# Kernel tuning notes

Measured on AMD Instinct MI355X. Metric: run time of the kernel, lower is better.

The kernel has to match this reference:

```python
import jax, jax.numpy as jnp
import numpy as np
import math

IN_CH = 512
OUT_CH = 512
KSIZE = 3
W_DIM = 512
CONV_SCALE = 1.0 / math.sqrt(IN_CH * KSIZE * KSIZE)
MOD_SCALE = 1.0 / math.sqrt(W_DIM)


def setup_inputs() -> dict:
    key = jax.random.key(0)
    k1, k2, k3, k4 = jax.random.split(key, 4)
    B, H, W = 16, 64, 64
    return {
        "input": jax.random.normal(k1, (B, IN_CH, H, W), dtype=jnp.float32),
        "style": jax.random.normal(k2, (B, W_DIM), dtype=jnp.float32),
        "weight": jax.random.normal(k3, (1, OUT_CH, IN_CH, KSIZE, KSIZE), dtype=jnp.float32),
        "mod_weight": jax.random.normal(k4, (IN_CH, W_DIM), dtype=jnp.float32),
        "mod_bias": jnp.ones((IN_CH,), dtype=jnp.float32),
    }


def reference(input, style, weight, mod_weight, mod_bias):
    B, Cin, H, Wd = input.shape
    # EqualLinear modulation: style -> per-sample, per-input-channel scale
    s = style @ (mod_weight * MOD_SCALE).T + mod_bias  # [B, Cin]
    s = s[:, None, :, None, None]                      # [B,1,Cin,1,1]
    w = CONV_SCALE * weight * s                        # [B,Cout,Cin,k,k]
    demod = jax.lax.rsqrt(jnp.sum(w * w, axis=(2, 3, 4)) + 1e-8)  # [B,Cout]
    w = w * demod[:, :, None, None, None]
    # Grouped conv with groups=batch, same as torch F.conv2d
    w = w.reshape(B * OUT_CH, Cin, KSIZE, KSIZE)
    x = input.reshape(1, B * Cin, H, Wd)
    pad = KSIZE // 2
    out = jax.lax.conv_general_dilated(
        x, w,
        window_strides=(1, 1),
        padding=[(pad, pad), (pad, pad)],
        dimension_numbers=("NCHW", "OIHW", "NCHW"),
        feature_group_count=B,
    )
    return out.reshape(B, OUT_CH, out.shape[2], out.shape[3])
```

## Files before the change

kernel.cpp:

```cpp
#include <hip/hip_runtime.h>
#include <hip/hip_bf16.h>


constexpr float CONV_SCALE = 0.014731391274719738f;
constexpr float MOD_SCALE  = 0.04419417382415922f;

typedef short  bf16x8 __attribute__((ext_vector_type(8)));
typedef float  f32x4  __attribute__((ext_vector_type(4)));

__device__ __forceinline__ unsigned short f2bf(float f) {
  unsigned u = __float_as_uint(f);
  u += 0x7fffu + ((u >> 16) & 1u);
  return (unsigned short)(u >> 16);
}

__device__ __forceinline__ void async16(const void* g, void* l) {
  __builtin_amdgcn_global_load_lds((const __attribute__((address_space(1))) unsigned int*)g,
                                   (__attribute__((address_space(3))) unsigned int*)l,
                                   16, 0, 0);
}

__global__ void k_style(const float* __restrict__ style, const float* __restrict__ mw,
                        const float* __restrict__ mb, float* __restrict__ s) {
  int t = blockIdx.x * 256 + threadIdx.x;
  int b = t & 15, i = t >> 4;
  const float* st = style + b * 512;
  const float* wr = mw + i * 512;
  float acc = 0.f;
  for (int j = 0; j < 512; ++j) acc += st[j] * wr[j];
  s[b * 512 + i] = acc * MOD_SCALE + mb[i];
}

__global__ void k_prepw(const float* __restrict__ w, float* __restrict__ wsq,
                        unsigned short* __restrict__ wt) {
  int t = blockIdx.x * 256 + threadIdx.x;
  int ic = t & 511, o = t >> 9;
  const float* wp = w + (size_t)(o * 512 + ic) * 9;
  float ssq = 0.f;
#pragma unroll
  for (int tap = 0; tap < 9; ++tap) {
    float v = wp[tap];
    ssq += v * v;
    wt[((size_t)tap * 512 + o) * 512 + ic] = f2bf(v);
  }
  wsq[o * 512 + ic] = ssq;
}

__global__ void k_dscale(const float* __restrict__ s, const float* __restrict__ wsq,
                         float* __restrict__ dscale) {
  int t = blockIdx.x * 256 + threadIdx.x;
  int b = t & 15, o = t >> 4;
  const float* sq = wsq + o * 512;
  const float* sb = s + b * 512;
  float acc = 0.f;
  for (int i = 0; i < 512; ++i) { float si = sb[i]; acc += sq[i] * si * si; }
  float d = rsqrtf(CONV_SCALE * CONV_SCALE * acc + 1e-8f);
  dscale[b * 512 + o] = d * CONV_SCALE;
}

__global__ void k_xt(const float* __restrict__ x, const float* __restrict__ s,
                     unsigned short* __restrict__ xt) {
  __shared__ float T[64][65];
  int h = blockIdx.x, b = blockIdx.y;
  const float* xp = x + (size_t)b * 512 * 4096 + h * 64;
  unsigned short* xo = xt + ((size_t)(b * 64 + h) * 64) * 512;
  int t = threadIdx.x;
  int wcol = t & 63, icl0 = t >> 6;
  for (int ic0 = 0; ic0 < 512; ic0 += 64) {
#pragma unroll
    for (int k = 0; k < 16; ++k) {
      int icl = icl0 + k * 4;
      int ic = ic0 + icl;
      T[icl][wcol] = xp[(size_t)ic * 4096 + wcol] * s[b * 512 + ic];
    }
    __syncthreads();
#pragma unroll
    for (int c = t; c < 512; c += 256) {
      int wv = c >> 3, ig = (c & 7) * 8;
      unsigned p0 = (unsigned)f2bf(T[ig + 0][wv]) | ((unsigned)f2bf(T[ig + 1][wv]) << 16);
      unsigned p1 = (unsigned)f2bf(T[ig + 2][wv]) | ((unsigned)f2bf(T[ig + 3][wv]) << 16);
      unsigned p2 = (unsigned)f2bf(T[ig + 4][wv]) | ((unsigned)f2bf(T[ig + 5][wv]) << 16);
      unsigned p3 = (unsigned)f2bf(T[ig + 6][wv]) | ((unsigned)f2bf(T[ig + 7][wv]) << 16);
      uint4 pk = {p0, p1, p2, p3};
      *(uint4*)&xo[(size_t)wv * 512 + ic0 + ig] = pk;
    }
    __syncthreads();
  }
}

__global__ __launch_bounds__(256, 3)
void k_conv(const unsigned short* __restrict__ xt, const unsigned short* __restrict__ wt,
            const float* __restrict__ dscale, float* __restrict__ out) {
  __shared__ short Xs[4 * 66 * 32];
  __shared__ short Ws[3 * 128 * 32];

  const int b  = blockIdx.z;
  const int o0 = blockIdx.y * 128;
  const int h0 = blockIdx.x * 2;
  const int t = threadIdx.x;
  const int wave = t >> 6, lane = t & 63;
  const int q = lane >> 4, l16 = lane & 15;
  const int wm = wave >> 1, wn = wave & 1;

  f32x4 acc[4][4];
#pragma unroll
  for (int i = 0; i < 4; ++i)
#pragma unroll
    for (int j = 0; j < 4; ++j) acc[i][j] = (f32x4){0.f, 0.f, 0.f, 0.f};

  {
    int r = t >> 6, c = (t >> 5) & 1, ch = t & 31;
    Xs[(r * 66 + c * 65) * 32 + ch] = 0;
  }

  const int hg = h0 - 1 + wave;
  const bool valid = (hg >= 0) && (hg < 64);
  const unsigned short* xrow =
      xt + ((size_t)(b * 64 + (valid ? hg : 0)) * 64) * 512 + (lane >> 2) * 512 + (lane & 3) * 8;

  for (int ic0 = 0; ic0 < 512; ic0 += 32) {
    __syncthreads();
    if (valid) {
#pragma unroll
      for (int j = 0; j < 4; ++j)
        async16(xrow + (size_t)j * 16 * 512 + ic0, &Xs[(wave * 66 + 1 + j * 16) * 32]);
    } else {
#pragma unroll
      for (int j = 0; j < 4; ++j)
        *(int4*)&Xs[(wave * 66 + 1 + j * 16) * 32 + lane * 8] = (int4){0, 0, 0, 0};
    }
#pragma unroll
    for (int kh = 0; kh < 3; ++kh) {
      if (kh) __syncthreads();
#pragma unroll
      for (int j = 0; j < 6; ++j) {
        int ci = wave * 6 + j;
        int kw = ci >> 3, oo = ((ci & 7) << 4) + (lane >> 2);
        async16(wt + (((size_t)(kh * 3 + kw) * 512 + o0 + oo) * 512 + ic0 + (lane & 3) * 8),
                &Ws[ci * 512]);
      }
      __syncthreads();
      const short* xbase = &Xs[(wn + kh) * 66 * 32 + q * 8];
#pragma unroll
      for (int kw = 0; kw < 3; ++kw) {
        bf16x8 af[4], bfr[4];
#pragma unroll
        for (int mi = 0; mi < 4; ++mi)
          af[mi] = *(const bf16x8*)&Ws[(kw * 128 + wm * 64 + mi * 16 + l16) * 32 + q * 8];
#pragma unroll
        for (int ni = 0; ni < 4; ++ni)
          bfr[ni] = *(const bf16x8*)&xbase[(ni * 16 + l16 + kw) * 32];
#pragma unroll
        for (int mi = 0; mi < 4; ++mi)
#pragma unroll
          for (int ni = 0; ni < 4; ++ni)
            acc[mi][ni] = __builtin_amdgcn_mfma_f32_16x16x32_bf16(af[mi], bfr[ni], acc[mi][ni], 0, 0, 0);
      }
    }
  }

  const int h = h0 + wn;
  float* orow = out + ((size_t)(b * 512 + o0 + wm * 64) * 64 + h) * 64;
#pragma unroll
  for (int mi = 0; mi < 4; ++mi) {
#pragma unroll
    for (int r = 0; r < 4; ++r) {
      int o_l = mi * 16 + q * 4 + r;
      float ds = dscale[b * 512 + o0 + wm * 64 + o_l];
#pragma unroll
      for (int ni = 0; ni < 4; ++ni)
        orow[(size_t)o_l * 4096 + ni * 16 + l16] = acc[mi][ni][r] * ds;
    }
  }
}

extern "C" void kernel_launch(void* const* d_in, const int* in_sizes, int n_in,
                              void* d_out, int out_size, void* d_ws, size_t ws_size,
                              hipStream_t stream) {
  const float* x      = (const float*)d_in[0];
  const float* style  = (const float*)d_in[1];
  const float* weight = (const float*)d_in[2];
  const float* mw     = (const float*)d_in[3];
  const float* mb     = (const float*)d_in[4];
  float* out = (float*)d_out;

  float* s      = (float*)d_ws;
  float* dscale = s + 8192;
  float* wsq    = dscale + 8192;
  unsigned short* wt = (unsigned short*)(wsq + 262144);
  unsigned short* xt = wt + 9 * 512 * 512;

  k_style<<<32, 256, 0, stream>>>(style, mw, mb, s);
  k_prepw<<<1024, 256, 0, stream>>>(weight, wsq, wt);
  k_dscale<<<32, 256, 0, stream>>>(s, wsq, dscale);
  k_xt<<<dim3(64, 16), 256, 0, stream>>>(x, s, xt);
  k_conv<<<dim3(32, 4, 16), 256, 0, stream>>>(xt, wt, dscale, out);
}
```

Baseline: 571.6 us.

## Enlarge conv tile to four output rows per block and vectorize prep kernels

The conv kernel now computes four output rows per block, with each wave owning one row and all 128 output channels. This raises reuse of the weight tiles staged in LDS and halves the number of blocks. The cost is a larger accumulator (32 f32x4 per wave), more LDS for the input halo and a lower occupancy bound. The style, dscale, xt and prepw kernels also use float4 loads, and prepw stages its weights through shared memory so global reads coalesce.

Result: faster. 516.1 us (-9.7%).

```diff
diff --git a/kernel.cpp b/kernel.cpp
--- a/kernel.cpp
+++ b/kernel.cpp
@@ -24,22 +24,34 @@
                         const float* __restrict__ mb, float* __restrict__ s) {
   int t = blockIdx.x * 256 + threadIdx.x;
   int b = t & 15, i = t >> 4;
-  const float* st = style + b * 512;
-  const float* wr = mw + i * 512;
+  const float4* st = (const float4*)(style + b * 512);
+  const float4* wr = (const float4*)(mw + i * 512);
   float acc = 0.f;
-  for (int j = 0; j < 512; ++j) acc += st[j] * wr[j];
+#pragma unroll 8
+  for (int j = 0; j < 128; ++j) {
+    float4 a = st[j], w4 = wr[j];
+    acc += a.x * w4.x + a.y * w4.y + a.z * w4.z + a.w * w4.w;
+  }
   s[b * 512 + i] = acc * MOD_SCALE + mb[i];
 }
 
 __global__ void k_prepw(const float* __restrict__ w, float* __restrict__ wsq,
                         unsigned short* __restrict__ wt) {
-  int t = blockIdx.x * 256 + threadIdx.x;
-  int ic = t & 511, o = t >> 9;
-  const float* wp = w + (size_t)(o * 512 + ic) * 9;
+  __shared__ float Wl[2304];
+  int t = threadIdx.x;
+  size_t base = (size_t)blockIdx.x * 2304;
+#pragma unroll
+  for (int k = 0; k < 3; ++k) {
+    int idx = t + k * 256;
+    if (idx < 576) ((float4*)Wl)[idx] = ((const float4*)(w + base))[idx];
+  }
+  __syncthreads();
+  int g = blockIdx.x * 256 + t;
+  int ic = g & 511, o = g >> 9;
   float ssq = 0.f;
 #pragma unroll
   for (int tap = 0; tap < 9; ++tap) {
-    float v = wp[tap];
+    float v = Wl[t * 9 + tap];
     ssq += v * v;
     wt[((size_t)tap * 512 + o) * 512 + ic] = f2bf(v);
   }
@@ -50,28 +62,35 @@
                          float* __restrict__ dscale) {
   int t = blockIdx.x * 256 + threadIdx.x;
   int b = t & 15, o = t >> 4;
-  const float* sq = wsq + o * 512;
-  const float* sb = s + b * 512;
+  const float4* sq = (const float4*)(wsq + o * 512);
+  const float4* sb = (const float4*)(s + b * 512);
   float acc = 0.f;
-  for (int i = 0; i < 512; ++i) { float si = sb[i]; acc += sq[i] * si * si; }
+#pragma unroll 8
+  for (int j = 0; j < 128; ++j) {
+    float4 q4 = sq[j], s4 = sb[j];
+    acc += q4.x * s4.x * s4.x + q4.y * s4.y * s4.y + q4.z * s4.z * s4.z + q4.w * s4.w * s4.w;
+  }
   float d = rsqrtf(CONV_SCALE * CONV_SCALE * acc + 1e-8f);
   dscale[b * 512 + o] = d * CONV_SCALE;
 }
 
 __global__ void k_xt(const float* __restrict__ x, const float* __restrict__ s,
                      unsigned short* __restrict__ xt) {
-  __shared__ float T[64][65];
+  __shared__ float T[64][68];
   int h = blockIdx.x, b = blockIdx.y;
   const float* xp = x + (size_t)b * 512 * 4096 + h * 64;
   unsigned short* xo = xt + ((size_t)(b * 64 + h) * 64) * 512;
   int t = threadIdx.x;
-  int wcol = t & 63, icl0 = t >> 6;
   for (int ic0 = 0; ic0 < 512; ic0 += 64) {
 #pragma unroll
-    for (int k = 0; k < 16; ++k) {
-      int icl = icl0 + k * 4;
+    for (int k = 0; k < 4; ++k) {
+      int idx = t + k * 256;
+      int icl = idx >> 4, c4 = idx & 15;
       int ic = ic0 + icl;
-      T[icl][wcol] = xp[(size_t)ic * 4096 + wcol] * s[b * 512 + ic];
+      float4 v = *(const float4*)&xp[(size_t)ic * 4096 + c4 * 4];
+      float sc = s[b * 512 + ic];
+      v.x *= sc; v.y *= sc; v.z *= sc; v.w *= sc;
+      *(float4*)&T[icl][c4 * 4] = v;
     }
     __syncthreads();
 #pragma unroll
@@ -88,46 +107,57 @@
   }
 }
 
-__global__ __launch_bounds__(256, 3)
+__global__ __launch_bounds__(256, 2)
 void k_conv(const unsigned short* __restrict__ xt, const unsigned short* __restrict__ wt,
             const float* __restrict__ dscale, float* __restrict__ out) {
-  __shared__ short Xs[4 * 66 * 32];
+  __shared__ short Xs[6 * 66 * 32];
   __shared__ short Ws[3 * 128 * 32];
 
   const int b  = blockIdx.z;
   const int o0 = blockIdx.y * 128;
-  const int h0 = blockIdx.x * 2;
+  const int h0 = blockIdx.x * 4;
   const int t = threadIdx.x;
   const int wave = t >> 6, lane = t & 63;
   const int q = lane >> 4, l16 = lane & 15;
-  const int wm = wave >> 1, wn = wave & 1;
-
-  f32x4 acc[4][4];
-#pragma unroll
-  for (int i = 0; i < 4; ++i)
+
+  f32x4 acc[8][4];
+#pragma unroll
+  for (int i = 0; i < 8; ++i)
 #pragma unroll
     for (int j = 0; j < 4; ++j) acc[i][j] = (f32x4){0.f, 0.f, 0.f, 0.f};
 
-  {
-    int r = t >> 6, c = (t >> 5) & 1, ch = t & 31;
-    Xs[(r * 66 + c * 65) * 32 + ch] = 0;
-  }
-
-  const int hg = h0 - 1 + wave;
-  const bool valid = (hg >= 0) && (hg < 64);
-  const unsigned short* xrow =
-      xt + ((size_t)(b * 64 + (valid ? hg : 0)) * 64) * 512 + (lane >> 2) * 512 + (lane & 3) * 8;
+  if (t < 192) {
+    int r = t >> 5, rem = t & 31;
+    int col = (rem >> 4) * 65, ch2 = (rem & 15) * 2;
+    *(int*)&Xs[(r * 66 + col) * 32 + ch2] = 0;
+  }
+
+  int xrowi[6]; bool xval[6];
+#pragma unroll
+  for (int j = 0; j < 6; ++j) {
+    int c = wave * 6 + j;
+    int row = c >> 2;
+    int hg = h0 - 1 + row;
+    xval[j] = (hg >= 0) && (hg < 64);
+    xrowi[j] = c;
+    (void)xrowi;
+  }
 
   for (int ic0 = 0; ic0 < 512; ic0 += 32) {
     __syncthreads();
-    if (valid) {
-#pragma unroll
-      for (int j = 0; j < 4; ++j)
-        async16(xrow + (size_t)j * 16 * 512 + ic0, &Xs[(wave * 66 + 1 + j * 16) * 32]);
-    } else {
-#pragma unroll
-      for (int j = 0; j < 4; ++j)
-        *(int4*)&Xs[(wave * 66 + 1 + j * 16) * 32 + lane * 8] = (int4){0, 0, 0, 0};
+#pragma unroll
+    for (int j = 0; j < 6; ++j) {
+      int c = wave * 6 + j;
+      int row = c >> 2, q16 = c & 3;
+      int hg = h0 - 1 + row;
+      short* dst = &Xs[(row * 66 + 1 + q16 * 16) * 32];
+      if (xval[j]) {
+        const unsigned short* src =
+            xt + ((size_t)((b * 64 + hg) * 64) + q16 * 16 + (lane >> 2)) * 512 + ic0 + (lane & 3) * 8;
+        async16(src, dst);
+      } else {
+        *(int4*)&dst[lane * 8] = (int4){0, 0, 0, 0};
+      }
     }
 #pragma unroll
     for (int kh = 0; kh < 3; ++kh) {
@@ -140,36 +170,35 @@
                 &Ws[ci * 512]);
       }
       __syncthreads();
-      const short* xbase = &Xs[(wn + kh) * 66 * 32 + q * 8];
+      const short* xbase = &Xs[(wave + kh) * 66 * 32 + q * 8];
 #pragma unroll
       for (int kw = 0; kw < 3; ++kw) {
-        bf16x8 af[4], bfr[4];
-#pragma unroll
-        for (int mi = 0; mi < 4; ++mi)
-          af[mi] = *(const bf16x8*)&Ws[(kw * 128 + wm * 64 + mi * 16 + l16) * 32 + q * 8];
+        bf16x8 bfr[4];
 #pragma unroll
         for (int ni = 0; ni < 4; ++ni)
           bfr[ni] = *(const bf16x8*)&xbase[(ni * 16 + l16 + kw) * 32];
 #pragma unroll
-        for (int mi = 0; mi < 4; ++mi)
+        for (int mi = 0; mi < 8; ++mi) {
+          bf16x8 af = *(const bf16x8*)&Ws[(kw * 128 + mi * 16 + l16) * 32 + q * 8];
 #pragma unroll
           for (int ni = 0; ni < 4; ++ni)
-            acc[mi][ni] = __builtin_amdgcn_mfma_f32_16x16x32_bf16(af[mi], bfr[ni], acc[mi][ni], 0, 0, 0);
+            acc[mi][ni] = __builtin_amdgcn_mfma_f32_16x16x32_bf16(af, bfr[ni], acc[mi][ni], 0, 0, 0);
+        }
       }
     }
   }
 
-  const int h = h0 + wn;
-  float* orow = out + ((size_t)(b * 512 + o0 + wm * 64) * 64 + h) * 64;
-#pragma unroll
-  for (int mi = 0; mi < 4; ++mi) {
+  const int h = h0 + wave;
+#pragma unroll
+  for (int mi = 0; mi < 8; ++mi) {
 #pragma unroll
     for (int r = 0; r < 4; ++r) {
       int o_l = mi * 16 + q * 4 + r;
-      float ds = dscale[b * 512 + o0 + wm * 64 + o_l];
+      float ds = dscale[b * 512 + o0 + o_l];
+      float* orow = out + ((size_t)(b * 512 + o0 + o_l) * 64 + h) * 64;
 #pragma unroll
       for (int ni = 0; ni < 4; ++ni)
-        orow[(size_t)o_l * 4096 + ni * 16 + l16] = acc[mi][ni][r] * ds;
+        orow[ni * 16 + l16] = acc[mi][ni][r] * ds;
     }
   }
 }
@@ -194,5 +223,5 @@
   k_prepw<<<1024, 256, 0, stream>>>(weight, wsq, wt);
   k_dscale<<<32, 256, 0, stream>>>(s, wsq, dscale);
   k_xt<<<dim3(64, 16), 256, 0, stream>>>(x, s, xt);
-  k_conv<<<dim3(32, 4, 16), 256, 0, stream>>>(xt, wt, dscale, out);
-}
+  k_conv<<<dim3(16, 4, 16), 256, 0, stream>>>(xt, wt, dscale, out);
+}
```
